# Kernel tuning notes

Measured on AMD Instinct MI355X. Metric: run time of the kernel, lower is better.

## Reference

```python
import jax, jax.numpy as jnp
import numpy as np
import math

N_HEADS = 8
LN_EPS = 1e-5

def _layernorm(x, g, b):
    m = jnp.mean(x, axis=-1, keepdims=True)
    v = jnp.var(x, axis=-1, keepdims=True)
    return (x - m) / jnp.sqrt(v + LN_EPS) * g + b

def _elu_feature(x):
    return jax.nn.elu(x) + 1.0

def _recurrence(Q, K, V, decay, reverse):
    # Q,K,V: (B,H,T,d); decay: (H,)
    B, H, T, d = Q.shape
    lamS = decay[None, :, None, None]
    lamz = decay[None, :, None]
    def step(carry, inp):
        S, z = carry
        q, k, v = inp
        S = lamS * S + k[..., :, None] * v[..., None, :]       # (B,H,d,d)
        z = lamz * z + k                                        # (B,H,d)
        y_raw = jnp.einsum('bhd,bhde->bhe', q, S)
        c_raw = jnp.sum(q * z, axis=-1)
        qk = jnp.sum(q * k, axis=-1, keepdims=True)
        return (S, z), (y_raw - 0.5 * qk * v, c_raw - 0.5 * qk[..., 0])
    S0 = jnp.zeros((B, H, d, d), Q.dtype)
    z0 = jnp.zeros((B, H, d), Q.dtype)
    qs = jnp.moveaxis(Q, 2, 0)
    ks = jnp.moveaxis(K, 2, 0)
    vs = jnp.moveaxis(V, 2, 0)
    _, (Y, C) = jax.lax.scan(step, (S0, z0), (qs, ks, vs), reverse=reverse)
    return jnp.moveaxis(Y, 0, 2), jnp.moveaxis(C, 0, 2)  # (B,H,T,d),(B,H,T)

def setup_inputs() -> dict:
    B, T, D, F = 2, 2048, 512, 2048
    key = jax.random.key(0)
    ks = jax.random.split(key, 8)
    std = 0.02
    return {
        'x': jax.random.normal(ks[0], (B, T, D), jnp.float32),
        'mask': jnp.zeros((B, T), dtype=bool),
        'Wq': jax.random.normal(ks[1], (D, D), jnp.float32) * std,
        'Wk': jax.random.normal(ks[2], (D, D), jnp.float32) * std,
        'Wv': jax.random.normal(ks[3], (D, D), jnp.float32) * std,
        'Wo': jax.random.normal(ks[4], (D, D), jnp.float32) * std,
        'bo': jnp.zeros((D,), jnp.float32),
        'g1': jnp.ones((D,), jnp.float32),
        'b1': jnp.zeros((D,), jnp.float32),
        'g2': jnp.ones((D,), jnp.float32),
        'b2': jnp.zeros((D,), jnp.float32),
        'W1': jax.random.normal(ks[5], (F, D), jnp.float32) * std,
        'bf1': jnp.zeros((F,), jnp.float32),
        'W2': jax.random.normal(ks[6], (D, F), jnp.float32) * std,
        'bf2': jnp.zeros((D,), jnp.float32),
        'decay_logit': jnp.full((N_HEADS,), math.log(9.0), jnp.float32),
    }

def reference(x, mask, Wq, Wk, Wv, Wo, bo, g1, b1, g2, b2, W1, bf1, W2, bf2, decay_logit):
    B, T, D = x.shape
    H = N_HEADS
    hd = D // H
    residual = x
    xn = _layernorm(x, g1, b1)
    def proj(W):
        return jnp.einsum('btd,od->bto', xn, W).reshape(B, T, H, hd).transpose(0, 2, 1, 3)
    Q = _elu_feature(proj(Wq))
    K = _elu_feature(proj(Wk))
    V = proj(Wv)
    pad = (~mask).astype(x.dtype)[:, None, :, None]  # (B,1,T,1)
    K = K * pad
    V = V * pad
    decay = jax.nn.sigmoid(decay_logit)
    Yf, Cf = _recurrence(Q, K, V, decay, reverse=False)
    Yb, Cb = _recurrence(Q, K, V, decay, reverse=True)
    denom = jnp.clip((Cf + Cb)[..., None], 1e-6)
    out = (Yf + Yb) / denom                       # (B,H,T,d)
    out = out.transpose(0, 2, 1, 3).reshape(B, T, D)
    out = jnp.einsum('btd,od->bto', out, Wo) + bo
    x = residual + out
    h = _layernorm(x, g2, b2)
    ffn = jnp.einsum('btd,fd->btf', h, W1) + bf1
    ffn = jax.nn.gelu(ffn, approximate=False)
    ffn = jnp.einsum('btf,df->btd', ffn, W2) + bf2
    return x + ffn
```

## Files before the change

### kernel.cpp

```cpp
#include <hip/hip_runtime.h>
#include <math.h>

#define BB 2
#define TT 2048
#define DD 512
#define FF 2048
#define HH 8
#define BT 4096
#define NC 32
#define CK 64

typedef __bf16 bf16_t;
typedef bf16_t bf16x8 __attribute__((ext_vector_type(8)));
typedef bf16_t bf16x4 __attribute__((ext_vector_type(4)));
typedef float f32x4 __attribute__((ext_vector_type(4)));

typedef const __attribute__((address_space(1))) void* gas_p;
typedef __attribute__((address_space(3))) void* las_p;

__device__ __forceinline__ void async16(const void* g, void* l) {
  __builtin_amdgcn_global_load_lds((gas_p)g, (las_p)l, 16, 0, 0);
}

#define PIPE_SYNC(vm) asm volatile("s_waitcnt lgkmcnt(0) vmcnt(" vm ")\n\ts_barrier" ::: "memory")

__global__ __launch_bounds__(256) void ln_cast_kernel(
    const float* __restrict__ x, const float* __restrict__ g, const float* __restrict__ bb,
    bf16_t* __restrict__ out,
    const float* __restrict__ Wq, const float* __restrict__ Wk,
    const float* __restrict__ Wv, const float* __restrict__ Wo,
    const float* __restrict__ W1, const float* __restrict__ W2,
    bf16_t* __restrict__ wdst) {
  int t = threadIdx.x;
  if (blockIdx.x >= BT) {
    size_t i = ((size_t)(blockIdx.x - BT) * 256 + t) * 8;
    const float* src; size_t off;
    if (i < 262144)       { src = Wq; off = i; }
    else if (i < 524288)  { src = Wk; off = i - 262144; }
    else if (i < 786432)  { src = Wv; off = i - 524288; }
    else if (i < 1048576) { src = Wo; off = i - 786432; }
    else if (i < 2097152) { src = W1; off = i - 1048576; }
    else                  { src = W2; off = i - 2097152; }
    float4 a = *(const float4*)(src + off);
    float4 b = *(const float4*)(src + off + 4);
    bf16x8 o;
    o[0] = (bf16_t)a.x; o[1] = (bf16_t)a.y; o[2] = (bf16_t)a.z; o[3] = (bf16_t)a.w;
    o[4] = (bf16_t)b.x; o[5] = (bf16_t)b.y; o[6] = (bf16_t)b.z; o[7] = (bf16_t)b.w;
    *(bf16x8*)(wdst + i) = o;
    return;
  }
  int row = blockIdx.x;
  const float* xr = x + (size_t)row * DD;
  float v0 = xr[t], v1 = xr[t + 256];
  float s = v0 + v1, sq = v0 * v0 + v1 * v1;
  for (int o = 32; o; o >>= 1) { s += __shfl_down(s, o); sq += __shfl_down(sq, o); }
  __shared__ float red[8];
  __shared__ float mv[2];
  int w = t >> 6;
  if ((t & 63) == 0) { red[w] = s; red[4 + w] = sq; }
  __syncthreads();
  if (t == 0) {
    float S = red[0] + red[1] + red[2] + red[3];
    float Q = red[4] + red[5] + red[6] + red[7];
    float m = S * (1.f / 512.f);
    float var = Q * (1.f / 512.f) - m * m;
    mv[0] = m; mv[1] = rsqrtf(var + 1e-5f);
  }
  __syncthreads();
  float m = mv[0], r = mv[1];
  out[(size_t)row * DD + t]       = (bf16_t)((v0 - m) * r * g[t] + bb[t]);
  out[(size_t)row * DD + t + 256] = (bf16_t)((v1 - m) * r * g[t + 256] + bb[t + 256]);
}

__global__ __launch_bounds__(256) void ln2_kernel(
    const float* __restrict__ x2, const float* __restrict__ g, const float* __restrict__ bb,
    bf16_t* __restrict__ out) {
  int row = blockIdx.x;
  int t = threadIdx.x;
  const float* xr = x2 + (size_t)row * DD;
  float v0 = xr[t], v1 = xr[t + 256];
  float s = v0 + v1, sq = v0 * v0 + v1 * v1;
  for (int o = 32; o; o >>= 1) { s += __shfl_down(s, o); sq += __shfl_down(sq, o); }
  __shared__ float red[8];
  __shared__ float mv[2];
  int w = t >> 6;
  if ((t & 63) == 0) { red[w] = s; red[4 + w] = sq; }
  __syncthreads();
  if (t == 0) {
    float S = red[0] + red[1] + red[2] + red[3];
    float Q = red[4] + red[5] + red[6] + red[7];
    float m = S * (1.f / 512.f);
    float var = Q * (1.f / 512.f) - m * m;
    mv[0] = m; mv[1] = rsqrtf(var + 1e-5f);
  }
  __syncthreads();
  float m = mv[0], r = mv[1];
  out[(size_t)row * DD + t]       = (bf16_t)((v0 - m) * r * g[t] + bb[t]);
  out[(size_t)row * DD + t + 256] = (bf16_t)((v1 - m) * r * g[t + 256] + bb[t + 256]);
}

template<int MODE>
__global__ __launch_bounds__(256) void mfma_gemm(
    const bf16_t* __restrict__ A, const bf16_t* __restrict__ B, int K, int NT,
    bf16_t* __restrict__ Qo, bf16_t* __restrict__ Ko, bf16_t* __restrict__ Vo,
    bf16_t* __restrict__ Ob, const float* __restrict__ bias,
    const unsigned char* __restrict__ mask) {
  __shared__ __align__(16) bf16_t smem[3 * 8192];
  int tid = threadIdx.x;
  int bid = blockIdx.x;
  int xcd = bid & 7;
  int tmp = bid >> 3;
  int nt = tmp % NT;
  int mt = (tmp / NT) * 8 + xcd;
  int n0 = nt * 128, m0 = mt * 128;
  int elt = tid * 8;
  int srow = elt >> 5, scol = elt & 31;
  const bf16_t* Ag = A + (size_t)(m0 + srow) * K + scol;
  const bf16_t* Bg = B + (size_t)(n0 + srow) * K + scol;
  size_t hstep = (size_t)64 * K;
  int NS = K >> 5;
#define ISSUE(s) { bf16_t* st = smem + ((s) % 3) * 8192; int k0 = (s) * 32; \
    async16(Ag + k0, st + elt); async16(Ag + k0 + hstep, st + 2048 + elt); \
    async16(Bg + k0, st + 4096 + elt); async16(Bg + k0 + hstep, st + 6144 + elt); }
  ISSUE(0); ISSUE(1);
  f32x4 acc[4][4] = {};
  int w = tid >> 6, l = tid & 63;
  int wm = (w >> 1) * 64, wn = (w & 1) * 64;
  int fr = l & 15, fk = (l >> 4) * 8;
  for (int i = 0; i < NS; i++) {
    if (i < NS - 1) PIPE_SYNC("4");
    else            PIPE_SYNC("0");
    if (i + 2 < NS) ISSUE(i + 2);
    const bf16_t* As = smem + (i % 3) * 8192;
    const bf16_t* Bs = As + 4096;
    bf16x8 af[4], bfr[4];
#pragma unroll
    for (int ii = 0; ii < 4; ii++) af[ii] = *(const bf16x8*)&As[(wm + ii * 16 + fr) * 32 + fk];
#pragma unroll
    for (int j = 0; j < 4; j++) bfr[j] = *(const bf16x8*)&Bs[(wn + j * 16 + fr) * 32 + fk];
#pragma unroll
    for (int ii = 0; ii < 4; ii++)
#pragma unroll
      for (int j = 0; j < 4; j++)
        acc[ii][j] = __builtin_amdgcn_mfma_f32_16x16x32_bf16(af[ii], bfr[j], acc[ii][j], 0, 0, 0);
  }
#undef ISSUE
  __syncthreads();
  const int CST = 136;
  int cn = l & 15, cr = (l >> 4) * 4;
  bf16_t* outp;
  int ldc, ncol0;
  if (MODE == 0) {
    int seg = n0 >> 9;
    outp = seg == 0 ? Qo : (seg == 1 ? Ko : Vo);
    ldc = 512; ncol0 = n0 & 511;
  } else {
    outp = Ob; ldc = 2048; ncol0 = n0;
  }
#pragma unroll
  for (int i = 0; i < 4; i++) {
#pragma unroll
    for (int r = 0; r < 4; r++) {
      int mrow = wm + i * 16 + cr + r;
      float p = 1.f;
      if (MODE == 0) p = mask[m0 + mrow] ? 0.f : 1.f;
#pragma unroll
      for (int j = 0; j < 4; j++) {
        int ncol = wn + j * 16 + cn;
        float v = acc[i][j][r];
        float ov;
        if (MODE == 0) {
          int seg = n0 >> 9;
          float e = v > 0.f ? v + 1.f : expf(v);
          ov = seg == 0 ? e : (seg == 1 ? e * p : v * p);
        } else {
          float t2 = v + bias[ncol0 + ncol];
          ov = 0.5f * t2 * (1.f + erff(t2 * 0.70710678118654752f));
        }
        smem[mrow * CST + ncol] = (bf16_t)ov;
      }
    }
  }
  __syncthreads();
#pragma unroll
  for (int it = 0; it < 8; it++) {
    int vec = tid + it * 256;
    int row = vec >> 4;
    int col = (vec & 15) * 8;
    bf16x8 v8 = *(const bf16x8*)&smem[row * CST + col];
    *(bf16x8*)(outp + (size_t)(m0 + row) * ldc + ncol0 + col) = v8;
  }
}

template<int MODE>
__global__ __launch_bounds__(256) void gemm64(
    const bf16_t* __restrict__ A, const bf16_t* __restrict__ B, int K, int NT,
    bf16_t* __restrict__ Qo, bf16_t* __restrict__ Ko, bf16_t* __restrict__ Vo,
    const float* __restrict__ bias, const float* __restrict__ resid,
    float* __restrict__ fout, const unsigned char* __restrict__ mask) {
  __shared__ __align__(16) bf16_t smem[4 * 6144];
  int tid = threadIdx.x;
  int bid = blockIdx.x;
  int xcd = bid & 7;
  int tmp = bid >> 3;
  int nt = tmp % NT;
  int mt = (tmp / NT) * 8 + xcd;
  int n0 = nt * 64, m0 = mt * 128;
  int elt = tid * 8;
  int srow = elt >> 5, scol = elt & 31;
  const bf16_t* Ag = A + (size_t)(m0 + srow) * K + scol;
  const bf16_t* Bg = B + (size_t)(n0 + srow) * K + scol;
  size_t hstep = (size_t)64 * K;
  const int NS = K >> 5;
#define ISSUE(s) { bf16_t* st = smem + ((s) & 3) * 6144; int k0 = (s) * 32; \
    async16(Ag + k0, st + elt); async16(Ag + k0 + hstep, st + 2048 + elt); \
    async16(Bg + k0, st + 4096 + elt); }
  ISSUE(0); ISSUE(1); ISSUE(2);
  f32x4 acc[4][2] = {};
  int w = tid >> 6, l = tid & 63;
  int wm = (w >> 1) * 64, wn = (w & 1) * 32;
  int fr = l & 15, fk = (l >> 4) * 8;
  for (int i = 0; i < NS; i++) {
    int rem = NS - 1 - i;
    if (rem >= 2)      PIPE_SYNC("6");
    else if (rem == 1) PIPE_SYNC("3");
    else               PIPE_SYNC("0");
    if (i + 3 < NS) ISSUE(i + 3);
    const bf16_t* As = smem + (i & 3) * 6144;
    const bf16_t* Bs = As + 4096;
    bf16x8 af[4], bfr[2];
#pragma unroll
    for (int ii = 0; ii < 4; ii++) af[ii] = *(const bf16x8*)&As[(wm + ii * 16 + fr) * 32 + fk];
#pragma unroll
    for (int j = 0; j < 2; j++) bfr[j] = *(const bf16x8*)&Bs[(wn + j * 16 + fr) * 32 + fk];
#pragma unroll
    for (int ii = 0; ii < 4; ii++)
#pragma unroll
      for (int j = 0; j < 2; j++)
        acc[ii][j] = __builtin_amdgcn_mfma_f32_16x16x32_bf16(af[ii], bfr[j], acc[ii][j], 0, 0, 0);
  }
#undef ISSUE
  __syncthreads();
  int cn = l & 15, cr = (l >> 4) * 4;
  if (MODE == 0) {
    const int CST = 72;
    int seg = n0 >> 9;
#pragma unroll
    for (int i = 0; i < 4; i++) {
#pragma unroll
      for (int r = 0; r < 4; r++) {
        int mrow = wm + i * 16 + cr + r;
        float p = mask[m0 + mrow] ? 0.f : 1.f;
#pragma unroll
        for (int j = 0; j < 2; j++) {
          int ncol = wn + j * 16 + cn;
          float v = acc[i][j][r];
          float e = v > 0.f ? v + 1.f : expf(v);
          float ov = seg == 0 ? e : (seg == 1 ? e * p : v * p);
          smem[mrow * CST + ncol] = (bf16_t)ov;
        }
      }
    }
    __syncthreads();
    bf16_t* outp = seg == 0 ? Qo : (seg == 1 ? Ko : Vo);
    int ncol0 = n0 & 511;
#pragma unroll
    for (int it = 0; it < 4; it++) {
      int vec = tid + it * 256;
      int row = vec >> 3;
      int col = (vec & 7) * 8;
      bf16x8 v8 = *(const bf16x8*)&smem[row * CST + col];
      *(bf16x8*)(outp + (size_t)(m0 + row) * 512 + ncol0 + col) = v8;
    }
  } else {
    const int FST = 72;
    float* smf = (float*)smem;
#pragma unroll
    for (int i = 0; i < 4; i++)
#pragma unroll
      for (int r = 0; r < 4; r++) {
        int mrow = wm + i * 16 + cr + r;
#pragma unroll
        for (int j = 0; j < 2; j++) {
          int ncol = wn + j * 16 + cn;
          smf[mrow * FST + ncol] = acc[i][j][r];
        }
      }
    __syncthreads();
#pragma unroll
    for (int it = 0; it < 8; it++) {
      int vec = tid + it * 256;
      int row = vec >> 4;
      int col = (vec & 15) * 4;
      size_t gidx = (size_t)(m0 + row) * 512 + n0 + col;
      float4 v = *(const float4*)&smf[row * FST + col];
      float4 bi = *(const float4*)(bias + n0 + col);
      float4 rr = *(const float4*)(resid + gidx);
      *(float4*)(fout + gidx) = make_float4(v.x + bi.x + rr.x, v.y + bi.y + rr.y,
                                            v.z + bi.z + rr.z, v.w + bi.w + rr.w);
    }
  }
}

__global__ __launch_bounds__(256) void chunk_summary_kernel(
    const bf16_t* __restrict__ Kb, const bf16_t* __restrict__ Vb,
    const float* __restrict__ dl, bf16_t* __restrict__ Sst, float* __restrict__ zst) {
  int chunk = blockIdx.x, bh = blockIdx.y;
  int b = bh >> 3, h = bh & 7;
  int t0 = chunk * CK;
  int tid = threadIdx.x;
  __shared__ __align__(16) float Ks[64][64];
  __shared__ __align__(16) float Vs[64][64];
  __shared__ float pw[72];
  float lam = 1.f / (1.f + expf(-dl[h]));
  if (tid <= 64) pw[tid] = powf(lam, (float)tid);
  int lrow = tid >> 2, lq = tid & 3;
  for (int q = 0; q < 2; q++) {
    int c = lq * 16 + q * 8;
    size_t g = ((size_t)(b * TT + t0 + lrow)) * DD + (size_t)h * 64 + c;
    bf16x8 k8 = *(const bf16x8*)(Kb + g);
    bf16x8 v8 = *(const bf16x8*)(Vb + g);
#pragma unroll
    for (int u = 0; u < 8; u++) { Ks[lrow][c + u] = (float)k8[u]; Vs[lrow][c + u] = (float)v8[u]; }
  }
  __syncthreads();
  int e1 = tid & 63;
  int e2b = (tid >> 6) * 16;
  float af_[16], ab_[16];
#pragma unroll
  for (int r = 0; r < 16; r++) { af_[r] = 0.f; ab_[r] = 0.f; }
  float zf = 0.f, zb = 0.f;
  for (int j = 0; j < 64; j++) {
    float kj = Ks[j][e1];
    float kf = pw[63 - j] * kj;
    float kb2 = pw[j] * kj;
    if (tid < 64) { zf += kf; zb += kb2; }
#pragma unroll
    for (int rr = 0; rr < 16; rr += 4) {
      float4 v4 = *(const float4*)&Vs[j][e2b + rr];
      af_[rr]     += kf * v4.x;  ab_[rr]     += kb2 * v4.x;
      af_[rr + 1] += kf * v4.y;  ab_[rr + 1] += kb2 * v4.y;
      af_[rr + 2] += kf * v4.z;  ab_[rr + 2] += kb2 * v4.z;
      af_[rr + 3] += kf * v4.w;  ab_[rr + 3] += kb2 * v4.w;
    }
  }
  size_t bfr = ((size_t)bh * NC + chunk) * 4096;
  size_t bbr = (((size_t)16 + bh) * NC + chunk) * 4096;
#pragma unroll
  for (int r = 0; r < 16; r++) {
    Sst[bfr + (size_t)(e2b + r) * 64 + e1] = (bf16_t)af_[r];
    Sst[bbr + (size_t)(e2b + r) * 64 + e1] = (bf16_t)ab_[r];
  }
  if (tid < 64) {
    zst[((size_t)bh * NC + chunk) * 64 + tid] = zf;
    zst[(((size_t)16 + bh) * NC + chunk) * 64 + tid] = zb;
  }
}

__global__ __launch_bounds__(256) void scan_kernel(bf16_t* __restrict__ Sst,
                                                   float* __restrict__ zst,
                                                   const float* __restrict__ dl) {
  int sub = blockIdx.x;
  int bh  = blockIdx.y;
  int dir = blockIdx.z;
  int h = bh & 7;
  int tid = threadIdx.x;
  float lam = 1.f / (1.f + expf(-dl[h]));
  float lamC = powf(lam, 64.f);
  int elem = sub * 256 + tid;
  size_t base = ((size_t)dir * 16 + bh) * (size_t)NC * 4096 + elem;
  float s = 0.f;
  for (int g = 0; g < 4; g++) {
    bf16_t L[8];
#pragma unroll
    for (int i = 0; i < 8; i++) {
      int st = g * 8 + i;
      int c = dir ? (NC - 1 - st) : st;
      L[i] = Sst[base + (size_t)c * 4096];
    }
#pragma unroll
    for (int i = 0; i < 8; i++) {
      int st = g * 8 + i;
      int c = dir ? (NC - 1 - st) : st;
      s = s * lamC + (float)L[i];
      Sst[base + (size_t)c * 4096] = (bf16_t)s;
    }
  }
  if (sub == 0 && tid < 64) {
    size_t zb = ((size_t)dir * 16 + bh) * (size_t)NC * 64 + tid;
    float z = 0.f;
    for (int g = 0; g < 4; g++) {
      float zL[8];
#pragma unroll
      for (int i = 0; i < 8; i++) {
        int st = g * 8 + i;
        int c = dir ? (NC - 1 - st) : st;
        zL[i] = zst[zb + (size_t)c * 64];
      }
#pragma unroll
      for (int i = 0; i < 8; i++) {
        int st = g * 8 + i;
        int c = dir ? (NC - 1 - st) : st;
        z = z * lamC + zL[i];
        zst[zb + (size_t)c * 64] = z;
      }
    }
  }
}

#define AST 72
__global__ __launch_bounds__(256) void chunk_attn_kernel(
    const bf16_t* __restrict__ Qb, const bf16_t* __restrict__ Kb, const bf16_t* __restrict__ Vb,
    const bf16_t* __restrict__ Sst, const float* __restrict__ zst, const float* __restrict__ dl,
    bf16_t* __restrict__ attnb) {
  int chunk = blockIdx.x, bh = blockIdx.y;
  int b = bh >> 3, h = bh & 7;
  int t0 = chunk * CK;
  int tid = threadIdx.x;
  __shared__ __align__(16) bf16_t Qa[64 * AST];
  __shared__ __align__(16) bf16_t KA[64 * AST];
  __shared__ __align__(16) bf16_t Vt[64 * AST];
  __shared__ __align__(16) bf16_t Sft[64 * AST];
  __shared__ __align__(16) bf16_t Sbt[64 * AST];
  __shared__ float rowpart[64][16];
  __shared__ float zpf[64], zpb[64];
  __shared__ float den[64];
  __shared__ float pw[72];
  float lam = 1.f / (1.f + expf(-dl[h]));
  if (tid <= 64) pw[tid] = powf(lam, (float)tid);
  int lrow = tid >> 2, lq = tid & 3;
  for (int q = 0; q < 2; q++) {
    int c = lq * 16 + q * 8;
    size_t g = ((size_t)(b * TT + t0 + lrow)) * DD + (size_t)h * 64 + c;
    bf16x8 q8 = *(const bf16x8*)(Qb + g);
    bf16x8 k8 = *(const bf16x8*)(Kb + g);
    bf16x8 v8 = *(const bf16x8*)(Vb + g);
    *(bf16x8*)&Qa[lrow * AST + c] = q8;
    *(bf16x8*)&KA[lrow * AST + c] = k8;
#pragma unroll
    for (int u = 0; u < 8; u++) Vt[(c + u) * AST + lrow] = v8[u];
  }
  {
    int c16 = lq * 16;
    if (chunk > 0) {
      const bf16_t* src = Sst + ((size_t)bh * NC + chunk - 1) * 4096 + (size_t)lrow * 64 + c16;
      *(bf16x8*)&Sft[lrow * AST + c16] = *(const bf16x8*)src;
      *(bf16x8*)&Sft[lrow * AST + c16 + 8] = *(const bf16x8*)(src + 8);
      if (tid < 64) zpf[tid] = zst[((size_t)bh * NC + chunk - 1) * 64 + tid];
    } else {
      bf16x8 z8 = {};
      *(bf16x8*)&Sft[lrow * AST + c16] = z8;
      *(bf16x8*)&Sft[lrow * AST + c16 + 8] = z8;
      if (tid < 64) zpf[tid] = 0.f;
    }
    if (chunk < NC - 1) {
      const bf16_t* src = Sst + (((size_t)16 + bh) * NC + chunk + 1) * 4096 + (size_t)lrow * 64 + c16;
      *(bf16x8*)&Sbt[lrow * AST + c16] = *(const bf16x8*)src;
      *(bf16x8*)&Sbt[lrow * AST + c16 + 8] = *(const bf16x8*)(src + 8);
      if (tid < 64) zpb[tid] = zst[(((size_t)16 + bh) * NC + chunk + 1) * 64 + tid];
    } else {
      bf16x8 z8 = {};
      *(bf16x8*)&Sbt[lrow * AST + c16] = z8;
      *(bf16x8*)&Sbt[lrow * AST + c16 + 8] = z8;
      if (tid < 64) zpb[tid] = 0.f;
    }
  }
  __syncthreads();
  int w = tid >> 6, l = tid & 63;
  int fr = l & 15, fk = (l >> 4) * 8;
  int cr = (l >> 4) * 4, cn = l & 15;
  int ms = w * 16;
  bf16x8 qf0 = *(const bf16x8*)&Qa[(ms + fr) * AST + fk];
  bf16x8 qf1 = *(const bf16x8*)&Qa[(ms + fr) * AST + 32 + fk];
  f32x4 aqk[4] = {};
#pragma unroll
  for (int t = 0; t < 4; t++) {
    bf16x8 kf0 = *(const bf16x8*)&KA[(t * 16 + fr) * AST + fk];
    bf16x8 kf1 = *(const bf16x8*)&KA[(t * 16 + fr) * AST + 32 + fk];
    aqk[t] = __builtin_amdgcn_mfma_f32_16x16x32_bf16(qf0, kf0, aqk[t], 0, 0, 0);
    aqk[t] = __builtin_amdgcn_mfma_f32_16x16x32_bf16(qf1, kf1, aqk[t], 0, 0, 0);
  }
  __syncthreads();
  float rs[4] = {0.f, 0.f, 0.f, 0.f};
#pragma unroll
  for (int t = 0; t < 4; t++) {
#pragma unroll
    for (int r = 0; r < 4; r++) {
      int i = ms + cr + r;
      int j = t * 16 + cn;
      int dd = i > j ? i - j : j - i;
      float v = aqk[t][r] * pw[dd];
      rs[r] += v;
      KA[i * AST + j] = (bf16_t)v;
    }
  }
#pragma unroll
  for (int r = 0; r < 4; r++) rowpart[ms + cr + r][cn] = rs[r];
  __syncthreads();
  bf16x8 af0 = *(const bf16x8*)&KA[(ms + fr) * AST + fk];
  bf16x8 af1 = *(const bf16x8*)&KA[(ms + fr) * AST + 32 + fk];
  f32x4 aY[4] = {}, aSf[4] = {}, aSb[4] = {};
#pragma unroll
  for (int t = 0; t < 4; t++) {
    bf16x8 vf0 = *(const bf16x8*)&Vt[(t * 16 + fr) * AST + fk];
    bf16x8 vf1 = *(const bf16x8*)&Vt[(t * 16 + fr) * AST + 32 + fk];
    aY[t] = __builtin_amdgcn_mfma_f32_16x16x32_bf16(af0, vf0, aY[t], 0, 0, 0);
    aY[t] = __builtin_amdgcn_mfma_f32_16x16x32_bf16(af1, vf1, aY[t], 0, 0, 0);
    bf16x8 sf0 = *(const bf16x8*)&Sft[(t * 16 + fr) * AST + fk];
    bf16x8 sf1 = *(const bf16x8*)&Sft[(t * 16 + fr) * AST + 32 + fk];
    aSf[t] = __builtin_amdgcn_mfma_f32_16x16x32_bf16(qf0, sf0, aSf[t], 0, 0, 0);
    aSf[t] = __builtin_amdgcn_mfma_f32_16x16x32_bf16(qf1, sf1, aSf[t], 0, 0, 0);
    bf16x8 sb0 = *(const bf16x8*)&Sbt[(t * 16 + fr) * AST + fk];
    bf16x8 sb1 = *(const bf16x8*)&Sbt[(t * 16 + fr) * AST + 32 + fk];
    aSb[t] = __builtin_amdgcn_mfma_f32_16x16x32_bf16(qf0, sb0, aSb[t], 0, 0, 0);
    aSb[t] = __builtin_amdgcn_mfma_f32_16x16x32_bf16(qf1, sb1, aSb[t], 0, 0, 0);
  }
  if (tid < 64) {
    int i = tid;
    float s = 0.f;
#pragma unroll
    for (int xx = 0; xx < 16; xx++) s += rowpart[i][xx];
    float czf = 0.f, czb = 0.f;
    for (int c = 0; c < 64; c += 8) {
      bf16x8 q8 = *(const bf16x8*)&Qa[i * AST + c];
#pragma unroll
      for (int u = 0; u < 8; u++) { czf += (float)q8[u] * zpf[c + u]; czb += (float)q8[u] * zpb[c + u]; }
    }
    den[i] = s + pw[i + 1] * czf + pw[64 - i] * czb;
  }
  __syncthreads();
#pragma unroll
  for (int t = 0; t < 4; t++) {
#pragma unroll
    for (int r = 0; r < 4; r++) {
      int i = ms + cr + r;
      int e = t * 16 + cn;
      float lrf = pw[i + 1], lrb = pw[64 - i];
      float inv = 1.f / fmaxf(den[i], 1e-6f);
      float val = (aY[t][r] + lrf * aSf[t][r] + lrb * aSb[t][r]) * inv;
      attnb[((size_t)(b * TT + t0 + i)) * DD + (size_t)h * 64 + e] = (bf16_t)val;
    }
  }
}

extern "C" void kernel_launch(void* const* d_in, const int* in_sizes, int n_in,
                              void* d_out, int out_size, void* d_ws, size_t ws_size,
                              hipStream_t stream) {
  const float* x   = (const float*)d_in[0];
  const unsigned char* mask = (const unsigned char*)d_in[1];
  const float* Wq  = (const float*)d_in[2];
  const float* Wk  = (const float*)d_in[3];
  const float* Wv  = (const float*)d_in[4];
  const float* Wo  = (const float*)d_in[5];
  const float* bo  = (const float*)d_in[6];
  const float* g1  = (const float*)d_in[7];
  const float* b1  = (const float*)d_in[8];
  const float* g2  = (const float*)d_in[9];
  const float* b2  = (const float*)d_in[10];
  const float* W1  = (const float*)d_in[11];
  const float* bf1 = (const float*)d_in[12];
  const float* W2  = (const float*)d_in[13];
  const float* bf2 = (const float*)d_in[14];
  const float* dl  = (const float*)d_in[15];
  float* out = (float*)d_out;

  float* ws = (float*)d_ws;
  const size_t U = (size_t)BT * DD;
  float* Qr  = ws;
  float* Kr  = ws + U;
  float* Vr  = ws + 2 * U;
  float* R3  = ws + 3 * U;
  float* R4  = ws + 4 * U;
  float* x2  = ws + 5 * U;
  bf16_t* Sstb = (bf16_t*)(ws + 6 * U);
  float* zst = ws + 8 * U;
  bf16_t* wall = (bf16_t*)(ws + 8 * U + 131072);
  bf16_t* Qb    = (bf16_t*)Qr;
  bf16_t* Kb    = (bf16_t*)Kr;
  bf16_t* Vb    = (bf16_t*)Vr;
  bf16_t* xnb   = (bf16_t*)R3;
  bf16_t* attnb = (bf16_t*)R4;
  bf16_t* h2b   = (bf16_t*)Qr;
  bf16_t* ffn1b = (bf16_t*)Kr;
  bf16_t* Wob = wall + 786432;
  bf16_t* W1b = wall + 1048576;
  bf16_t* W2b = wall + 2097152;

  ln_cast_kernel<<<BT + 1536, 256, 0, stream>>>(x, g1, b1, xnb, Wq, Wk, Wv, Wo, W1, W2, wall);
  gemm64<0><<<768, 256, 0, stream>>>(xnb, wall, 512, 24, Qb, Kb, Vb,
                                     nullptr, nullptr, nullptr, mask);
  chunk_summary_kernel<<<dim3(NC, 16), 256, 0, stream>>>(Kb, Vb, dl, Sstb, zst);
  scan_kernel<<<dim3(16, 16, 2), 256, 0, stream>>>(Sstb, zst, dl);
  chunk_attn_kernel<<<dim3(NC, 16), 256, 0, stream>>>(Qb, Kb, Vb, Sstb, zst, dl, attnb);
  gemm64<1><<<256, 256, 0, stream>>>(attnb, Wob, 512, 8, nullptr, nullptr, nullptr,
                                     bo, x, x2, nullptr);
  ln2_kernel<<<BT, 256, 0, stream>>>(x2, g2, b2, h2b);
  mfma_gemm<2><<<512, 256, 0, stream>>>(h2b, W1b, 512, 16, nullptr, nullptr, nullptr,
                                        ffn1b, bf1, nullptr);
  gemm64<1><<<256, 256, 0, stream>>>(ffn1b, W2b, 2048, 8, nullptr, nullptr, nullptr,
                                     bf2, x2, out, nullptr);
}
```

Before: 192.7 us.

## Use MFMA for chunk summaries, wave-per-row layernorm, parallel denominator reduction

The chunk summary kernel now pre-scales K by the decay powers into transposed bf16 tiles and computes the forward and backward K^T V states with bf16 MFMA instead of scalar FP32 loops. It writes the results back through shared memory so the global stores are coalesced. Both layernorm kernels now handle one row per wave, using vectorized loads and xor-shuffle reductions with no block barriers. The attention denominator is now computed by all 256 threads, with shuffle reduction, instead of 64. The trade-off is lower precision for the state summaries: decay-weighted K and the summaries are rounded to bf16 before and after the MFMA.

```diff
diff --git a/kernel.cpp b/kernel.cpp
--- a/kernel.cpp
+++ b/kernel.cpp
@@ -32,8 +32,8 @@
     const float* __restrict__ W1, const float* __restrict__ W2,
     bf16_t* __restrict__ wdst) {
   int t = threadIdx.x;
-  if (blockIdx.x >= BT) {
-    size_t i = ((size_t)(blockIdx.x - BT) * 256 + t) * 8;
+  if (blockIdx.x >= 1024) {
+    size_t i = ((size_t)(blockIdx.x - 1024) * 256 + t) * 8;
     const float* src; size_t off;
     if (i < 262144)       { src = Wq; off = i; }
     else if (i < 524288)  { src = Wk; off = i - 262144; }
@@ -49,54 +49,62 @@
     *(bf16x8*)(wdst + i) = o;
     return;
   }
-  int row = blockIdx.x;
-  const float* xr = x + (size_t)row * DD;
-  float v0 = xr[t], v1 = xr[t + 256];
-  float s = v0 + v1, sq = v0 * v0 + v1 * v1;
-  for (int o = 32; o; o >>= 1) { s += __shfl_down(s, o); sq += __shfl_down(sq, o); }
-  __shared__ float red[8];
-  __shared__ float mv[2];
-  int w = t >> 6;
-  if ((t & 63) == 0) { red[w] = s; red[4 + w] = sq; }
-  __syncthreads();
-  if (t == 0) {
-    float S = red[0] + red[1] + red[2] + red[3];
-    float Q = red[4] + red[5] + red[6] + red[7];
-    float m = S * (1.f / 512.f);
-    float var = Q * (1.f / 512.f) - m * m;
-    mv[0] = m; mv[1] = rsqrtf(var + 1e-5f);
-  }
-  __syncthreads();
-  float m = mv[0], r = mv[1];
-  out[(size_t)row * DD + t]       = (bf16_t)((v0 - m) * r * g[t] + bb[t]);
-  out[(size_t)row * DD + t + 256] = (bf16_t)((v1 - m) * r * g[t + 256] + bb[t + 256]);
+  int w = t >> 6, l = t & 63;
+  int row = blockIdx.x * 4 + w;
+  int c0 = l * 8;
+  const float* xr = x + (size_t)row * DD + c0;
+  float4 a = *(const float4*)xr;
+  float4 b4 = *(const float4*)(xr + 4);
+  float s  = a.x + a.y + a.z + a.w + b4.x + b4.y + b4.z + b4.w;
+  float sq = a.x*a.x + a.y*a.y + a.z*a.z + a.w*a.w +
+             b4.x*b4.x + b4.y*b4.y + b4.z*b4.z + b4.w*b4.w;
+  for (int o = 32; o; o >>= 1) { s += __shfl_xor(s, o); sq += __shfl_xor(sq, o); }
+  float m = s * (1.f / 512.f);
+  float var = sq * (1.f / 512.f) - m * m;
+  float r = rsqrtf(var + 1e-5f);
+  float4 ga = *(const float4*)(g + c0);  float4 gb = *(const float4*)(g + c0 + 4);
+  float4 ba = *(const float4*)(bb + c0); float4 bbv = *(const float4*)(bb + c0 + 4);
+  bf16x8 o8;
+  o8[0] = (bf16_t)((a.x - m) * r * ga.x + ba.x);
+  o8[1] = (bf16_t)((a.y - m) * r * ga.y + ba.y);
+  o8[2] = (bf16_t)((a.z - m) * r * ga.z + ba.z);
+  o8[3] = (bf16_t)((a.w - m) * r * ga.w + ba.w);
+  o8[4] = (bf16_t)((b4.x - m) * r * gb.x + bbv.x);
+  o8[5] = (bf16_t)((b4.y - m) * r * gb.y + bbv.y);
+  o8[6] = (bf16_t)((b4.z - m) * r * gb.z + bbv.z);
+  o8[7] = (bf16_t)((b4.w - m) * r * gb.w + bbv.w);
+  *(bf16x8*)(out + (size_t)row * DD + c0) = o8;
 }
 
 __global__ __launch_bounds__(256) void ln2_kernel(
     const float* __restrict__ x2, const float* __restrict__ g, const float* __restrict__ bb,
     bf16_t* __restrict__ out) {
-  int row = blockIdx.x;
   int t = threadIdx.x;
-  const float* xr = x2 + (size_t)row * DD;
-  float v0 = xr[t], v1 = xr[t + 256];
-  float s = v0 + v1, sq = v0 * v0 + v1 * v1;
-  for (int o = 32; o; o >>= 1) { s += __shfl_down(s, o); sq += __shfl_down(sq, o); }
-  __shared__ float red[8];
-  __shared__ float mv[2];
-  int w = t >> 6;
-  if ((t & 63) == 0) { red[w] = s; red[4 + w] = sq; }
-  __syncthreads();
-  if (t == 0) {
-    float S = red[0] + red[1] + red[2] + red[3];
-    float Q = red[4] + red[5] + red[6] + red[7];
-    float m = S * (1.f / 512.f);
-    float var = Q * (1.f / 512.f) - m * m;
-    mv[0] = m; mv[1] = rsqrtf(var + 1e-5f);
-  }
-  __syncthreads();
-  float m = mv[0], r = mv[1];
-  out[(size_t)row * DD + t]       = (bf16_t)((v0 - m) * r * g[t] + bb[t]);
-  out[(size_t)row * DD + t + 256] = (bf16_t)((v1 - m) * r * g[t + 256] + bb[t + 256]);
+  int w = t >> 6, l = t & 63;
+  int row = blockIdx.x * 4 + w;
+  int c0 = l * 8;
+  const float* xr = x2 + (size_t)row * DD + c0;
+  float4 a = *(const float4*)xr;
+  float4 b4 = *(const float4*)(xr + 4);
+  float s  = a.x + a.y + a.z + a.w + b4.x + b4.y + b4.z + b4.w;
+  float sq = a.x*a.x + a.y*a.y + a.z*a.z + a.w*a.w +
+             b4.x*b4.x + b4.y*b4.y + b4.z*b4.z + b4.w*b4.w;
+  for (int o = 32; o; o >>= 1) { s += __shfl_xor(s, o); sq += __shfl_xor(sq, o); }
+  float m = s * (1.f / 512.f);
+  float var = sq * (1.f / 512.f) - m * m;
+  float r = rsqrtf(var + 1e-5f);
+  float4 ga = *(const float4*)(g + c0);  float4 gb = *(const float4*)(g + c0 + 4);
+  float4 ba = *(const float4*)(bb + c0); float4 bbv = *(const float4*)(bb + c0 + 4);
+  bf16x8 o8;
+  o8[0] = (bf16_t)((a.x - m) * r * ga.x + ba.x);
+  o8[1] = (bf16_t)((a.y - m) * r * ga.y + ba.y);
+  o8[2] = (bf16_t)((a.z - m) * r * ga.z + ba.z);
+  o8[3] = (bf16_t)((a.w - m) * r * ga.w + ba.w);
+  o8[4] = (bf16_t)((b4.x - m) * r * gb.x + bbv.x);
+  o8[5] = (bf16_t)((b4.y - m) * r * gb.y + bbv.y);
+  o8[6] = (bf16_t)((b4.z - m) * r * gb.z + bbv.z);
+  o8[7] = (bf16_t)((b4.w - m) * r * gb.w + bbv.w);
+  *(bf16x8*)(out + (size_t)row * DD + c0) = o8;
 }
 
 template<int MODE>
@@ -309,51 +317,88 @@
   int b = bh >> 3, h = bh & 7;
   int t0 = chunk * CK;
   int tid = threadIdx.x;
-  __shared__ __align__(16) float Ks[64][64];
-  __shared__ __align__(16) float Vs[64][64];
-  __shared__ float pw[72];
+  const int ST = 72;
+  __shared__ __align__(16) bf16_t KTf[64 * ST];
+  __shared__ __align__(16) bf16_t KTb[64 * ST];
+  __shared__ __align__(16) bf16_t VT [64 * ST];
   float lam = 1.f / (1.f + expf(-dl[h]));
-  if (tid <= 64) pw[tid] = powf(lam, (float)tid);
   int lrow = tid >> 2, lq = tid & 3;
+  float wf = powf(lam, (float)(63 - lrow));
+  float wb = powf(lam, (float)lrow);
+#pragma unroll
   for (int q = 0; q < 2; q++) {
     int c = lq * 16 + q * 8;
-    size_t g = ((size_t)(b * TT + t0 + lrow)) * DD + (size_t)h * 64 + c;
-    bf16x8 k8 = *(const bf16x8*)(Kb + g);
-    bf16x8 v8 = *(const bf16x8*)(Vb + g);
-#pragma unroll
-    for (int u = 0; u < 8; u++) { Ks[lrow][c + u] = (float)k8[u]; Vs[lrow][c + u] = (float)v8[u]; }
-  }
-  __syncthreads();
-  int e1 = tid & 63;
-  int e2b = (tid >> 6) * 16;
-  float af_[16], ab_[16];
-#pragma unroll
-  for (int r = 0; r < 16; r++) { af_[r] = 0.f; ab_[r] = 0.f; }
-  float zf = 0.f, zb = 0.f;
-  for (int j = 0; j < 64; j++) {
-    float kj = Ks[j][e1];
-    float kf = pw[63 - j] * kj;
-    float kb2 = pw[j] * kj;
-    if (tid < 64) { zf += kf; zb += kb2; }
-#pragma unroll
-    for (int rr = 0; rr < 16; rr += 4) {
-      float4 v4 = *(const float4*)&Vs[j][e2b + rr];
-      af_[rr]     += kf * v4.x;  ab_[rr]     += kb2 * v4.x;
-      af_[rr + 1] += kf * v4.y;  ab_[rr + 1] += kb2 * v4.y;
-      af_[rr + 2] += kf * v4.z;  ab_[rr + 2] += kb2 * v4.z;
-      af_[rr + 3] += kf * v4.w;  ab_[rr + 3] += kb2 * v4.w;
-    }
-  }
+    size_t gidx = ((size_t)(b * TT + t0 + lrow)) * DD + (size_t)h * 64 + c;
+    bf16x8 k8 = *(const bf16x8*)(Kb + gidx);
+    bf16x8 v8 = *(const bf16x8*)(Vb + gidx);
+#pragma unroll
+    for (int u = 0; u < 8; u++) {
+      float kv = (float)k8[u];
+      KTf[(c + u) * ST + lrow] = (bf16_t)(kv * wf);
+      KTb[(c + u) * ST + lrow] = (bf16_t)(kv * wb);
+      VT [(c + u) * ST + lrow] = v8[u];
+    }
+  }
+  __syncthreads();
+  int w = tid >> 6, l = tid & 63;
+  int dir = w >> 1;
+  int drow = (w & 1) * 32;
+  const bf16_t* KT = dir ? KTb : KTf;
+  int fr = l & 15, fk = (l >> 4) * 8;
+  bf16x8 afrag[2][2], bfrag[4][2];
+#pragma unroll
+  for (int ti = 0; ti < 2; ti++) {
+    afrag[ti][0] = *(const bf16x8*)&KT[(drow + ti * 16 + fr) * ST + fk];
+    afrag[ti][1] = *(const bf16x8*)&KT[(drow + ti * 16 + fr) * ST + 32 + fk];
+  }
+#pragma unroll
+  for (int tj = 0; tj < 4; tj++) {
+    bfrag[tj][0] = *(const bf16x8*)&VT[(tj * 16 + fr) * ST + fk];
+    bfrag[tj][1] = *(const bf16x8*)&VT[(tj * 16 + fr) * ST + 32 + fk];
+  }
+  f32x4 acc[2][4] = {};
+#pragma unroll
+  for (int ti = 0; ti < 2; ti++)
+#pragma unroll
+    for (int tj = 0; tj < 4; tj++) {
+      acc[ti][tj] = __builtin_amdgcn_mfma_f32_16x16x32_bf16(afrag[ti][0], bfrag[tj][0], acc[ti][tj], 0, 0, 0);
+      acc[ti][tj] = __builtin_amdgcn_mfma_f32_16x16x32_bf16(afrag[ti][1], bfrag[tj][1], acc[ti][tj], 0, 0, 0);
+    }
+  if (tid < 128) {
+    const bf16_t* KTz = (tid >> 6) ? KTb : KTf;
+    int d = tid & 63;
+    float z = 0.f;
+    for (int j = 0; j < 64; j += 8) {
+      bf16x8 kz = *(const bf16x8*)&KTz[d * ST + j];
+#pragma unroll
+      for (int u = 0; u < 8; u++) z += (float)kz[u];
+    }
+    zst[(((size_t)(tid >> 6) * 16 + bh) * NC + chunk) * 64 + d] = z;
+  }
+  __syncthreads();
+  bf16_t* Ss = dir ? KTb : KTf;
+  int cr = (l >> 4) * 4, cn = l & 15;
+#pragma unroll
+  for (int ti = 0; ti < 2; ti++)
+#pragma unroll
+    for (int tj = 0; tj < 4; tj++)
+#pragma unroll
+      for (int r = 0; r < 4; r++) {
+        int d = drow + ti * 16 + cr + r;
+        int e = tj * 16 + cn;
+        Ss[e * ST + d] = (bf16_t)acc[ti][tj][r];
+      }
+  __syncthreads();
   size_t bfr = ((size_t)bh * NC + chunk) * 4096;
   size_t bbr = (((size_t)16 + bh) * NC + chunk) * 4096;
 #pragma unroll
-  for (int r = 0; r < 16; r++) {
-    Sst[bfr + (size_t)(e2b + r) * 64 + e1] = (bf16_t)af_[r];
-    Sst[bbr + (size_t)(e2b + r) * 64 + e1] = (bf16_t)ab_[r];
-  }
-  if (tid < 64) {
-    zst[((size_t)bh * NC + chunk) * 64 + tid] = zf;
-    zst[(((size_t)16 + bh) * NC + chunk) * 64 + tid] = zb;
+  for (int it = 0; it < 4; it++) {
+    int vec = tid + it * 256;
+    int d2 = vec >> 9;
+    int idx = vec & 511;
+    int row = idx >> 3, col = (idx & 7) * 8;
+    bf16x8 v8 = *(const bf16x8*)((d2 ? KTb : KTf) + row * ST + col);
+    *(bf16x8*)(Sst + (d2 ? bbr : bfr) + (size_t)row * 64 + col) = v8;
   }
 }
 
@@ -515,18 +560,23 @@
     aSb[t] = __builtin_amdgcn_mfma_f32_16x16x32_bf16(qf0, sb0, aSb[t], 0, 0, 0);
     aSb[t] = __builtin_amdgcn_mfma_f32_16x16x32_bf16(qf1, sb1, aSb[t], 0, 0, 0);
   }
-  if (tid < 64) {
-    int i = tid;
+  {
+    int i = tid >> 2, p = tid & 3;
     float s = 0.f;
 #pragma unroll
-    for (int xx = 0; xx < 16; xx++) s += rowpart[i][xx];
+    for (int xx = 0; xx < 4; xx++) s += rowpart[i][p * 4 + xx];
     float czf = 0.f, czb = 0.f;
-    for (int c = 0; c < 64; c += 8) {
+#pragma unroll
+    for (int cc = 0; cc < 2; cc++) {
+      int c = p * 16 + cc * 8;
       bf16x8 q8 = *(const bf16x8*)&Qa[i * AST + c];
 #pragma unroll
       for (int u = 0; u < 8; u++) { czf += (float)q8[u] * zpf[c + u]; czb += (float)q8[u] * zpb[c + u]; }
     }
-    den[i] = s + pw[i + 1] * czf + pw[64 - i] * czb;
+    float dsum = s + pw[i + 1] * czf + pw[64 - i] * czb;
+    dsum += __shfl_xor(dsum, 1);
+    dsum += __shfl_xor(dsum, 2);
+    if (p == 0) den[i] = dsum;
   }
   __syncthreads();
 #pragma unroll
@@ -586,7 +636,7 @@
   bf16_t* W1b = wall + 1048576;
   bf16_t* W2b = wall + 2097152;
 
-  ln_cast_kernel<<<BT + 1536, 256, 0, stream>>>(x, g1, b1, xnb, Wq, Wk, Wv, Wo, W1, W2, wall);
+  ln_cast_kernel<<<1024 + 1536, 256, 0, stream>>>(x, g1, b1, xnb, Wq, Wk, Wv, Wo, W1, W2, wall);
   gemm64<0><<<768, 256, 0, stream>>>(xnb, wall, 512, 24, Qb, Kb, Vb,
                                      nullptr, nullptr, nullptr, mask);
   chunk_summary_kernel<<<dim3(NC, 16), 256, 0, stream>>>(Kb, Vb, dl, Sstb, zst);
@@ -594,7 +644,7 @@
   chunk_attn_kernel<<<dim3(NC, 16), 256, 0, stream>>>(Qb, Kb, Vb, Sstb, zst, dl, attnb);
   gemm64<1><<<256, 256, 0, stream>>>(attnb, Wob, 512, 8, nullptr, nullptr, nullptr,
                                      bo, x, x2, nullptr);
-  ln2_kernel<<<BT, 256, 0, stream>>>(x2, g2, b2, h2b);
+  ln2_kernel<<<1024, 256, 0, stream>>>(x2, g2, b2, h2b);
   mfma_gemm<2><<<512, 256, 0, stream>>>(h2b, W1b, 512, 16, nullptr, nullptr, nullptr,
                                         ffn1b, bf1, nullptr);
   gemm64<1><<<256, 256, 0, stream>>>(ffn1b, W2b, 2048, 8, nullptr, nullptr, nullptr,
```

Result: faster. 184.3 us (-4.4%).
